# Kernel optimization log

Hardware: AMD Instinct MI355X
Metric: run time of the kernel (lower is better)

Reference implementation:

```python
import jax, jax.numpy as jnp
import numpy as np

D_MODEL = 2048
D_FF = 4 * D_MODEL  # 8192, GPT-2 MLP convention
TOTAL = D_MODEL * D_FF          # elements per weight matrix
L = TOTAL // 2                  # complex FFT length (real/imag interleaved pairs)
NUM_COEFFS = 16
BATCH, SEQ = 2, 4096


def _decompress(coeffs_real, coeffs_imag, indices, shape, scale):
    """Faithful port of FastPoincareFourier.decompress_matrix.
    Scatter K complex coeffs into a length-L zero buffer, ifft, then
    de-interleave real/imag back into a flat real vector of length 2L == TOTAL.
    """
    coeffs = jax.lax.complex(coeffs_real, coeffs_imag)
    full_fft = jnp.zeros((L,), dtype=jnp.complex64).at[indices].set(coeffs)
    restored = jnp.fft.ifft(full_fft)  # [L] complex
    # stack([real, imag], dim=1).flatten() -> interleaved [2L]
    flat = jnp.stack([jnp.real(restored), jnp.imag(restored)], axis=1).reshape(-1)
    # 2L == TOTAL exactly (TOTAL is even), so no trunc/pad needed
    return flat.reshape(shape) * scale  # scale broadcasts ([1])


def setup_inputs() -> dict:
    key = jax.random.key(0)
    ks = jax.random.split(key, 12)
    # coefficients scaled by L*0.02 so ifft (which divides by L) yields ~N(0,0.02) weights
    cscale = L * 0.02
    return {
        "x": jax.random.normal(ks[0], (BATCH, SEQ, D_MODEL), dtype=jnp.float32),
        "fc_coeffs_real": jax.random.normal(ks[1], (NUM_COEFFS,), dtype=jnp.float32) * cscale,
        "fc_coeffs_imag": jax.random.normal(ks[2], (NUM_COEFFS,), dtype=jnp.float32) * cscale,
        "fc_scale": jax.random.uniform(ks[3], (1,), dtype=jnp.float32) + 0.5,
        "proj_coeffs_real": jax.random.normal(ks[4], (NUM_COEFFS,), dtype=jnp.float32) * cscale,
        "proj_coeffs_imag": jax.random.normal(ks[5], (NUM_COEFFS,), dtype=jnp.float32) * cscale,
        "proj_scale": jax.random.uniform(ks[6], (1,), dtype=jnp.float32) + 0.5,
        "c_fc_bias": jax.random.normal(ks[7], (D_FF,), dtype=jnp.float32) * 0.02,
        "c_proj_bias": jax.random.normal(ks[8], (D_MODEL,), dtype=jnp.float32) * 0.02,
        "fc_indices": jax.random.randint(ks[9], (NUM_COEFFS,), 0, L, dtype=jnp.int64),
        "proj_indices": jax.random.randint(ks[10], (NUM_COEFFS,), 0, L, dtype=jnp.int64),
    }


def reference(x, fc_coeffs_real, fc_coeffs_imag, fc_scale,
              proj_coeffs_real, proj_coeffs_imag, proj_scale,
              c_fc_bias, c_proj_bias, fc_indices, proj_indices):
    # W_fc: [d_model, d_ff]; F.linear(x, W.T) == x @ W
    w_fc = _decompress(fc_coeffs_real, fc_coeffs_imag, fc_indices, (D_MODEL, D_FF), fc_scale)
    h = jnp.einsum('bsd,df->bsf', x, w_fc) + c_fc_bias
    h = jax.nn.gelu(h, approximate=False)  # nn.GELU() default = exact erf
    # W_proj: [d_ff, d_model]
    w_proj = _decompress(proj_coeffs_real, proj_coeffs_imag, proj_indices, (D_FF, D_MODEL), proj_scale)
    out = jnp.einsum('bsf,fd->bsd', h, w_proj) + c_proj_bias
    return out
```

## Files before the change

kernel.cpp:

```cpp
#include <hip/hip_runtime.h>
#include <stdint.h>


typedef short bfrag8 __attribute__((ext_vector_type(8)));
typedef short bfrag4 __attribute__((ext_vector_type(4)));
typedef float f32x4  __attribute__((ext_vector_type(4)));

#define LMASK 8388607u
#define TWO_PI_OVER_L 7.4901405658478575e-7f

__device__ __forceinline__ unsigned short f2bf(float f) {
    unsigned u = __float_as_uint(f);
    u = (u + 0x7FFFu + ((u >> 16) & 1u)) >> 16;
    return (unsigned short)u;
}
__device__ __forceinline__ float bf2f(unsigned short h) {
    unsigned u = ((unsigned)h) << 16;
    return __builtin_bit_cast(float, u);
}
__device__ __forceinline__ unsigned pk2bf(float a, float b) {
    unsigned ua = __float_as_uint(a) + 0x8000u;
    unsigned ub = __float_as_uint(b) + 0x8000u;
    return __builtin_amdgcn_perm(ub, ua, 0x07060302u);
}
__device__ __forceinline__ float gelu_fast(float x) {
    float xx = x * x;
    float p  = fmaf(xx, 0.044715f, 1.0f);
    float t  = (x * p) * -2.3022083f;
    float e  = __builtin_amdgcn_exp2f(t);
    return x * __builtin_amdgcn_rcpf(1.0f + e);
}
__device__ __forceinline__ void sc_ph(unsigned ph, float& sn, float& cs) {
    __sincosf((float)ph * TWO_PI_OVER_L, &sn, &cs);
}

#if defined(__has_builtin)
#if __has_builtin(__builtin_amdgcn_mfma_f32_16x16x16bf16_1k)
#define HAVE_MFMA16_1K 1
#endif
#endif
__device__ __forceinline__ void mfma16(f32x4& acc, bfrag4 a, bfrag4 b) {
#ifdef HAVE_MFMA16_1K
    acc = __builtin_amdgcn_mfma_f32_16x16x16bf16_1k(a, b, acc, 0, 0, 0);
#else
    asm("v_mfma_f32_16x16x16_bf16 %0, %1, %2, %0" : "+v"(acc) : "v"(a), "v"(b));
#endif
}

__device__ __forceinline__ bool keep_coef(const int* __restrict__ idx, int kk) {
    int v = idx[kk];
    bool keep = true;
    for (int j = kk + 1; j < 16; ++j) keep = keep && (idx[j] != v);
    return keep;
}

__global__ __launch_bounds__(512, 4) void k_t1(
    const float* __restrict__ x,
    const float* __restrict__ fcr, const float* __restrict__ fci,
    const int* __restrict__ fidx,  const float* __restrict__ fcs,
    unsigned short* __restrict__ t1)
{
    __shared__ float red[8 * 512];
    const int tid  = threadIdx.x;
    const int w    = tid >> 6;
    const int lane = tid & 63;
    const int lr   = lane & 15;
    const int hi   = lane >> 4;
    const size_t tok0 = (size_t)blockIdx.x * 16;

    const float sc = fcs[0] * (1.0f / 8388608.0f);
    const int p   = lr & 1;
    const int kk0 = lr >> 1, kk1 = 8 + (lr >> 1);
    unsigned s0, s1; float a0, b0, a1, b1;
    {
        bool k0 = keep_coef(fidx, kk0), k1 = keep_coef(fidx, kk1);
        s0 = (((unsigned)fidx[kk0]) << 12) & LMASK;
        s1 = (((unsigned)fidx[kk1]) << 12) & LMASK;
        a0 = k0 ? fcr[kk0] * sc : 0.f;  b0 = k0 ? fci[kk0] * sc : 0.f;
        a1 = k1 ? fcr[kk1] * sc : 0.f;  b1 = k1 ? fci[kk1] * sc : 0.f;
    }

    f32x4 acc[2];
    { f32x4 z = {0.f,0.f,0.f,0.f}; acc[0] = z; acc[1] = z; }
    #pragma unroll 2
    for (int s = 0; s < 8; ++s) {
        int k = w * 256 + s * 32 + hi * 8;
        const float* xp = x + (tok0 + lr) * 2048 + k;
        float4 v0 = *(const float4*)xp;
        float4 v1 = *(const float4*)(xp + 4);
        uint4 aw = make_uint4(pk2bf(v0.x, v0.y), pk2bf(v0.z, v0.w),
                              pk2bf(v1.x, v1.y), pk2bf(v1.z, v1.w));
        bfrag8 af = __builtin_bit_cast(bfrag8, aw);
        float e0[8], e1[8];
        #pragma unroll
        for (int t = 0; t < 8; ++t) {
            float sn, cs;
            sc_ph((s0 * (unsigned)(k + t)) & LMASK, sn, cs);
            e0[t] = p ? fmaf(a0, sn, b0 * cs) : fmaf(a0, cs, -b0 * sn);
            sc_ph((s1 * (unsigned)(k + t)) & LMASK, sn, cs);
            e1[t] = p ? fmaf(a1, sn, b1 * cs) : fmaf(a1, cs, -b1 * sn);
        }
        uint4 bw0 = make_uint4(pk2bf(e0[0], e0[1]), pk2bf(e0[2], e0[3]),
                               pk2bf(e0[4], e0[5]), pk2bf(e0[6], e0[7]));
        uint4 bw1 = make_uint4(pk2bf(e1[0], e1[1]), pk2bf(e1[2], e1[3]),
                               pk2bf(e1[4], e1[5]), pk2bf(e1[6], e1[7]));
        bfrag8 bf0 = __builtin_bit_cast(bfrag8, bw0);
        bfrag8 bf1 = __builtin_bit_cast(bfrag8, bw1);
        acc[0] = __builtin_amdgcn_mfma_f32_16x16x32_bf16(af, bf0, acc[0], 0, 0, 0);
        acc[1] = __builtin_amdgcn_mfma_f32_16x16x32_bf16(af, bf1, acc[1], 0, 0, 0);
    }
    #pragma unroll
    for (int nj = 0; nj < 2; ++nj)
        #pragma unroll
        for (int r = 0; r < 4; ++r)
            red[w * 512 + (hi * 4 + r) * 32 + nj * 16 + lr] = acc[nj][r];
    __syncthreads();
    float s = 0.f;
    #pragma unroll
    for (int w2 = 0; w2 < 8; ++w2) s += red[w2 * 512 + tid];
    t1[(size_t)blockIdx.x * 512 + tid] = f2bf(s);
}

__global__ __launch_bounds__(512, 4) void k_mid(
    const unsigned short* __restrict__ t1,
    const int* __restrict__ fidx,
    const int* __restrict__ pidx,
    const float* __restrict__ prr, const float* __restrict__ pri,
    const float* __restrict__ prs,
    const float* __restrict__ fcb,
    unsigned short* __restrict__ t2p)
{
    __shared__ float red[2 * 8 * 512];
    const int tid  = threadIdx.x;
    const int w    = tid >> 6;
    const int lane = tid & 63;
    const int lr   = lane & 15;
    const int hi   = lane >> 4;
    const int fc   = blockIdx.x;
    const int g0   = blockIdx.y * 16;
    const int fb_w = fc * 512 + w * 64;

    bfrag8 va0[2], va1[2];
    f32x4  cb0[2], cb1[2];
    unsigned skv[4];
    #pragma unroll
    for (int c = 0; c < 4; ++c) skv[c] = ((unsigned)fidx[hi * 4 + c]) & LMASK;
    #pragma unroll
    for (int sl = 0; sl < 2; ++sl) {
        #pragma unroll
        for (int rv = 0; rv < 2; ++rv) {
            int j = fb_w + sl * 32 + rv * 16 + lr;
            unsigned m = ((unsigned)j) >> 1;
            int pj = j & 1;
            float v[8];
            #pragma unroll
            for (int c = 0; c < 4; ++c) {
                float sn, cs;
                sc_ph((skv[c] * m) & LMASK, sn, cs);
                v[2 * c]     = pj ? sn : cs;
                v[2 * c + 1] = pj ? cs : -sn;
            }
            uint4 pw = make_uint4(pk2bf(v[0], v[1]), pk2bf(v[2], v[3]),
                                  pk2bf(v[4], v[5]), pk2bf(v[6], v[7]));
            if (rv == 0) va0[sl] = __builtin_bit_cast(bfrag8, pw);
            else         va1[sl] = __builtin_bit_cast(bfrag8, pw);
        }
        int fb = fb_w + sl * 32;
        cb0[sl] = *(const f32x4*)(fcb + fb + hi * 4);
        cb1[sl] = *(const f32x4*)(fcb + fb + 16 + hi * 4);
    }

    bfrag4 u00[2], u01[2], u10[2], u11[2];
    {
        const float scp = prs[0] * (1.0f / 8388608.0f);
        const int pp = lr & 1;
        #pragma unroll
        for (int rv = 0; rv < 2; ++rv) {
            int kk = rv * 8 + (lr >> 1);
            bool kp = keep_coef(pidx, kk);
            unsigned s = (((unsigned)pidx[kk]) << 10) & LMASK;
            float a = kp ? prr[kk] * scp : 0.f;
            float b = kp ? pri[kk] * scp : 0.f;
            #pragma unroll
            for (int sl = 0; sl < 2; ++sl) {
                #pragma unroll
                for (int hf = 0; hf < 2; ++hf) {
                    unsigned f0 = (unsigned)(fb_w + sl * 32 + hf * 16 + 4 * hi);
                    float v[4];
                    #pragma unroll
                    for (int t = 0; t < 4; ++t) {
                        float sn, cs;
                        sc_ph((s * (f0 + t)) & LMASK, sn, cs);
                        v[t] = pp ? fmaf(a, sn, b * cs) : fmaf(a, cs, -b * sn);
                    }
                    uint2 pw = make_uint2(pk2bf(v[0], v[1]), pk2bf(v[2], v[3]));
                    bfrag4 fr = __builtin_bit_cast(bfrag4, pw);
                    if      (rv == 0 && hf == 0) u00[sl] = fr;
                    else if (rv == 0 && hf == 1) u01[sl] = fr;
                    else if (rv == 1 && hf == 0) u10[sl] = fr;
                    else                         u11[sl] = fr;
                }
            }
        }
    }
    const int toff = lr * 32 + hi * 8;

    #pragma unroll 1
    for (int pi = 0; pi < 8; ++pi) {
        int ga = g0 + pi * 2, gb = ga + 1;
        bfrag8 tA = *(const bfrag8*)(t1 + (size_t)ga * 512 + toff);
        bfrag8 tB = *(const bfrag8*)(t1 + (size_t)gb * 512 + toff);
        f32x4 aA0 = {0.f,0.f,0.f,0.f}, aA1 = {0.f,0.f,0.f,0.f};
        f32x4 aB0 = {0.f,0.f,0.f,0.f}, aB1 = {0.f,0.f,0.f,0.f};
        #pragma unroll
        for (int sl = 0; sl < 2; ++sl) {
            f32x4 sA0 = __builtin_amdgcn_mfma_f32_16x16x32_bf16(va0[sl], tA, cb0[sl], 0, 0, 0);
            f32x4 sB0 = __builtin_amdgcn_mfma_f32_16x16x32_bf16(va0[sl], tB, cb0[sl], 0, 0, 0);
            f32x4 sA1 = __builtin_amdgcn_mfma_f32_16x16x32_bf16(va1[sl], tA, cb1[sl], 0, 0, 0);
            f32x4 sB1 = __builtin_amdgcn_mfma_f32_16x16x32_bf16(va1[sl], tB, cb1[sl], 0, 0, 0);
            uint2 hA0 = make_uint2(pk2bf(gelu_fast(sA0[0]), gelu_fast(sA0[1])),
                                   pk2bf(gelu_fast(sA0[2]), gelu_fast(sA0[3])));
            uint2 hB0 = make_uint2(pk2bf(gelu_fast(sB0[0]), gelu_fast(sB0[1])),
                                   pk2bf(gelu_fast(sB0[2]), gelu_fast(sB0[3])));
            uint2 hA1 = make_uint2(pk2bf(gelu_fast(sA1[0]), gelu_fast(sA1[1])),
                                   pk2bf(gelu_fast(sA1[2]), gelu_fast(sA1[3])));
            uint2 hB1 = make_uint2(pk2bf(gelu_fast(sB1[0]), gelu_fast(sB1[1])),
                                   pk2bf(gelu_fast(sB1[2]), gelu_fast(sB1[3])));
            bfrag4 fA0 = __builtin_bit_cast(bfrag4, hA0);
            bfrag4 fB0 = __builtin_bit_cast(bfrag4, hB0);
            bfrag4 fA1 = __builtin_bit_cast(bfrag4, hA1);
            bfrag4 fB1 = __builtin_bit_cast(bfrag4, hB1);
            mfma16(aA0, u00[sl], fA0);
            mfma16(aB0, u00[sl], fB0);
            mfma16(aA1, u10[sl], fA0);
            mfma16(aB1, u10[sl], fB0);
            mfma16(aA0, u01[sl], fA1);
            mfma16(aB0, u01[sl], fB1);
            mfma16(aA1, u11[sl], fA1);
            mfma16(aB1, u11[sl], fB1);
        }
        #pragma unroll
        for (int r = 0; r < 4; ++r) {
            int r2a = hi * 4 + r, r2b = 16 + hi * 4 + r;
            red[(0 * 8 + w) * 512 + lr * 32 + ((r2a + lr) & 31)] = aA0[r];
            red[(0 * 8 + w) * 512 + lr * 32 + ((r2b + lr) & 31)] = aA1[r];
            red[(1 * 8 + w) * 512 + lr * 32 + ((r2a + lr) & 31)] = aB0[r];
            red[(1 * 8 + w) * 512 + lr * 32 + ((r2b + lr) & 31)] = aB1[r];
        }
        __syncthreads();
        {
            int tok = tid >> 5, rr = tid & 31;
            int slot = tok * 32 + ((rr + tok) & 31);
            float sa = 0.f, sb = 0.f;
            #pragma unroll
            for (int w2 = 0; w2 < 8; ++w2) {
                sa += red[(0 * 8 + w2) * 512 + slot];
                sb += red[(1 * 8 + w2) * 512 + slot];
            }
            t2p[((size_t)fc * 512 + ga) * 512 + tid] = f2bf(sa);
            t2p[((size_t)fc * 512 + gb) * 512 + tid] = f2bf(sb);
        }
        __syncthreads();
    }
}

__global__ __launch_bounds__(512, 4) void k_out(
    const unsigned short* __restrict__ t2p,
    const int* __restrict__ pidx,
    const float* __restrict__ prb,
    float* __restrict__ out)
{
    __shared__ unsigned short lT[512];
    const int tid  = threadIdx.x;
    const int w    = tid >> 6;
    const int lane = tid & 63;
    const int lr   = lane & 15;
    const int hi   = lane >> 4;
    const int g    = blockIdx.x;
    const size_t tok0 = (size_t)g * 16;

    {
        float s = 0.f;
        #pragma unroll
        for (int c = 0; c < 16; ++c)
            s += bf2f(t2p[((size_t)c * 512 + g) * 512 + tid]);
        lT[tid] = f2bf(s);
    }
    unsigned skv[4];
    #pragma unroll
    for (int c = 0; c < 4; ++c) skv[c] = ((unsigned)pidx[hi * 4 + c]) & LMASK;
    __syncthreads();
    const bfrag8 t2a = *(const bfrag8*)(lT + lr * 32 + hi * 8);
    #pragma unroll 4
    for (int nj = 0; nj < 16; ++nj) {
        int d = w * 256 + nj * 16 + lr;
        unsigned m = ((unsigned)d) >> 1;
        int pd = d & 1;
        float v[8];
        #pragma unroll
        for (int c = 0; c < 4; ++c) {
            float sn, cs;
            sc_ph((skv[c] * m) & LMASK, sn, cs);
            v[2 * c]     = pd ? sn : cs;
            v[2 * c + 1] = pd ? cs : -sn;
        }
        uint4 pw = make_uint4(pk2bf(v[0], v[1]), pk2bf(v[2], v[3]),
                              pk2bf(v[4], v[5]), pk2bf(v[6], v[7]));
        bfrag8 vp = __builtin_bit_cast(bfrag8, pw);
        float bn = prb[d];
        f32x4 c4 = {bn, bn, bn, bn};
        f32x4 o = __builtin_amdgcn_mfma_f32_16x16x32_bf16(t2a, vp, c4, 0, 0, 0);
        #pragma unroll
        for (int r = 0; r < 4; ++r)
            out[(tok0 + hi * 4 + r) * 2048 + d] = o[r];
    }
}

extern "C" void kernel_launch(void* const* d_in, const int* in_sizes, int n_in,
                              void* d_out, int out_size, void* d_ws, size_t ws_size,
                              hipStream_t stream) {
    (void)in_sizes; (void)n_in; (void)out_size; (void)ws_size;
    const float* x   = (const float*)d_in[0];
    const float* fcr = (const float*)d_in[1];
    const float* fci = (const float*)d_in[2];
    const float* fcs = (const float*)d_in[3];
    const float* prr = (const float*)d_in[4];
    const float* pri = (const float*)d_in[5];
    const float* prs = (const float*)d_in[6];
    const float* fcb = (const float*)d_in[7];
    const float* prb = (const float*)d_in[8];
    const int* fidx  = (const int*)d_in[9];
    const int* pidx  = (const int*)d_in[10];
    float* out = (float*)d_out;
    char* ws = (char*)d_ws;

    size_t off = 0;
    auto take = [&](size_t bytes) { size_t p = off; off = (off + bytes + 255) & ~(size_t)255; return p; };
    unsigned short* t1  = (unsigned short*)(ws + take((size_t)8192 * 32 * 2));
    unsigned short* t2p = (unsigned short*)(ws + take((size_t)16 * 8192 * 32 * 2));

    k_t1 <<<dim3(512),    512, 0, stream>>>(x, fcr, fci, fidx, fcs, t1);
    k_mid<<<dim3(16, 32), 512, 0, stream>>>(t1, fidx, pidx, prr, pri, prs, fcb, t2p);
    k_out<<<dim3(512),    512, 0, stream>>>(t2p, pidx, prb, out);
}
```

Before: 76.90 us.

## Stage fc/proj basis in LDS and split tokens across waves in k_mid

k_mid now computes the fc and proj Fourier basis fragments once per block into shared memory, with padded rows. Each wave then owns two token groups and loops over all 512 ff columns, replacing the per-wave column split that needed a cross-wave LDS reduction and two barriers per iteration. This removes the reduction traffic and synchronisation. In exchange it adds LDS reads in the inner loop, uses more shared memory, and lowers the launch-bounds occupancy hint from 4 to 2.

```diff
diff --git a/kernel.cpp b/kernel.cpp
--- a/kernel.cpp
+++ b/kernel.cpp
@@ -121,7 +121,7 @@
     t1[(size_t)blockIdx.x * 512 + tid] = f2bf(s);
 }
 
-__global__ __launch_bounds__(512, 4) void k_mid(
+__global__ __launch_bounds__(512, 2) void k_mid(
     const unsigned short* __restrict__ t1,
     const int* __restrict__ fidx,
     const int* __restrict__ pidx,
@@ -130,137 +130,86 @@
     const float* __restrict__ fcb,
     unsigned short* __restrict__ t2p)
 {
-    __shared__ float red[2 * 8 * 512];
+    __shared__ __align__(16) unsigned short vfc[512 * 32];
+    __shared__ __align__(16) unsigned short upr[32 * 520];
+    __shared__ float lbias[512];
     const int tid  = threadIdx.x;
     const int w    = tid >> 6;
     const int lane = tid & 63;
     const int lr   = lane & 15;
     const int hi   = lane >> 4;
     const int fc   = blockIdx.x;
-    const int g0   = blockIdx.y * 16;
-    const int fb_w = fc * 512 + w * 64;
-
-    bfrag8 va0[2], va1[2];
-    f32x4  cb0[2], cb1[2];
-    unsigned skv[4];
-    #pragma unroll
-    for (int c = 0; c < 4; ++c) skv[c] = ((unsigned)fidx[hi * 4 + c]) & LMASK;
-    #pragma unroll
-    for (int sl = 0; sl < 2; ++sl) {
-        #pragma unroll
-        for (int rv = 0; rv < 2; ++rv) {
-            int j = fb_w + sl * 32 + rv * 16 + lr;
-            unsigned m = ((unsigned)j) >> 1;
-            int pj = j & 1;
-            float v[8];
-            #pragma unroll
-            for (int c = 0; c < 4; ++c) {
-                float sn, cs;
-                sc_ph((skv[c] * m) & LMASK, sn, cs);
-                v[2 * c]     = pj ? sn : cs;
-                v[2 * c + 1] = pj ? cs : -sn;
-            }
-            uint4 pw = make_uint4(pk2bf(v[0], v[1]), pk2bf(v[2], v[3]),
-                                  pk2bf(v[4], v[5]), pk2bf(v[6], v[7]));
-            if (rv == 0) va0[sl] = __builtin_bit_cast(bfrag8, pw);
-            else         va1[sl] = __builtin_bit_cast(bfrag8, pw);
-        }
-        int fb = fb_w + sl * 32;
-        cb0[sl] = *(const f32x4*)(fcb + fb + hi * 4);
-        cb1[sl] = *(const f32x4*)(fcb + fb + 16 + hi * 4);
-    }
-
-    bfrag4 u00[2], u01[2], u10[2], u11[2];
+
+    {
+        int jg = fc * 512 + tid;
+        unsigned m = ((unsigned)jg) >> 1;
+        int pj = jg & 1;
+        unsigned short* row = vfc + tid * 32;
+        #pragma unroll
+        for (int k = 0; k < 16; ++k) {
+            float sn, cs;
+            sc_ph(((((unsigned)fidx[k]) & LMASK) * m) & LMASK, sn, cs);
+            row[2 * k]     = f2bf(pj ? sn : cs);
+            row[2 * k + 1] = f2bf(pj ? cs : -sn);
+        }
+    }
     {
         const float scp = prs[0] * (1.0f / 8388608.0f);
-        const int pp = lr & 1;
-        #pragma unroll
-        for (int rv = 0; rv < 2; ++rv) {
-            int kk = rv * 8 + (lr >> 1);
-            bool kp = keep_coef(pidx, kk);
-            unsigned s = (((unsigned)pidx[kk]) << 10) & LMASK;
-            float a = kp ? prr[kk] * scp : 0.f;
-            float b = kp ? pri[kk] * scp : 0.f;
-            #pragma unroll
-            for (int sl = 0; sl < 2; ++sl) {
-                #pragma unroll
-                for (int hf = 0; hf < 2; ++hf) {
-                    unsigned f0 = (unsigned)(fb_w + sl * 32 + hf * 16 + 4 * hi);
-                    float v[4];
-                    #pragma unroll
-                    for (int t = 0; t < 4; ++t) {
-                        float sn, cs;
-                        sc_ph((s * (f0 + t)) & LMASK, sn, cs);
-                        v[t] = pp ? fmaf(a, sn, b * cs) : fmaf(a, cs, -b * sn);
-                    }
-                    uint2 pw = make_uint2(pk2bf(v[0], v[1]), pk2bf(v[2], v[3]));
-                    bfrag4 fr = __builtin_bit_cast(bfrag4, pw);
-                    if      (rv == 0 && hf == 0) u00[sl] = fr;
-                    else if (rv == 0 && hf == 1) u01[sl] = fr;
-                    else if (rv == 1 && hf == 0) u10[sl] = fr;
-                    else                         u11[sl] = fr;
-                }
-            }
-        }
-    }
+        int k  = tid >> 5;
+        int f0 = (tid & 31) * 16;
+        bool kp = keep_coef(pidx, k);
+        unsigned s = (((unsigned)pidx[k]) << 10) & LMASK;
+        float a = kp ? prr[k] * scp : 0.f;
+        float b = kp ? pri[k] * scp : 0.f;
+        unsigned short* r0 = upr + (2 * k) * 520 + f0;
+        unsigned short* r1 = upr + (2 * k + 1) * 520 + f0;
+        unsigned fg = (unsigned)(fc * 512 + f0);
+        #pragma unroll
+        for (int t = 0; t < 16; ++t) {
+            float sn, cs;
+            sc_ph((s * (fg + t)) & LMASK, sn, cs);
+            r0[t] = f2bf(fmaf(a, cs, -b * sn));
+            r1[t] = f2bf(fmaf(a, sn, b * cs));
+        }
+    }
+    lbias[tid] = fcb[fc * 512 + tid];
+    __syncthreads();
+
+    const int ga = blockIdx.y * 16 + w * 2, gb = ga + 1;
     const int toff = lr * 32 + hi * 8;
-
-    #pragma unroll 1
-    for (int pi = 0; pi < 8; ++pi) {
-        int ga = g0 + pi * 2, gb = ga + 1;
-        bfrag8 tA = *(const bfrag8*)(t1 + (size_t)ga * 512 + toff);
-        bfrag8 tB = *(const bfrag8*)(t1 + (size_t)gb * 512 + toff);
-        f32x4 aA0 = {0.f,0.f,0.f,0.f}, aA1 = {0.f,0.f,0.f,0.f};
-        f32x4 aB0 = {0.f,0.f,0.f,0.f}, aB1 = {0.f,0.f,0.f,0.f};
-        #pragma unroll
-        for (int sl = 0; sl < 2; ++sl) {
-            f32x4 sA0 = __builtin_amdgcn_mfma_f32_16x16x32_bf16(va0[sl], tA, cb0[sl], 0, 0, 0);
-            f32x4 sB0 = __builtin_amdgcn_mfma_f32_16x16x32_bf16(va0[sl], tB, cb0[sl], 0, 0, 0);
-            f32x4 sA1 = __builtin_amdgcn_mfma_f32_16x16x32_bf16(va1[sl], tA, cb1[sl], 0, 0, 0);
-            f32x4 sB1 = __builtin_amdgcn_mfma_f32_16x16x32_bf16(va1[sl], tB, cb1[sl], 0, 0, 0);
-            uint2 hA0 = make_uint2(pk2bf(gelu_fast(sA0[0]), gelu_fast(sA0[1])),
-                                   pk2bf(gelu_fast(sA0[2]), gelu_fast(sA0[3])));
-            uint2 hB0 = make_uint2(pk2bf(gelu_fast(sB0[0]), gelu_fast(sB0[1])),
-                                   pk2bf(gelu_fast(sB0[2]), gelu_fast(sB0[3])));
-            uint2 hA1 = make_uint2(pk2bf(gelu_fast(sA1[0]), gelu_fast(sA1[1])),
-                                   pk2bf(gelu_fast(sA1[2]), gelu_fast(sA1[3])));
-            uint2 hB1 = make_uint2(pk2bf(gelu_fast(sB1[0]), gelu_fast(sB1[1])),
-                                   pk2bf(gelu_fast(sB1[2]), gelu_fast(sB1[3])));
-            bfrag4 fA0 = __builtin_bit_cast(bfrag4, hA0);
-            bfrag4 fB0 = __builtin_bit_cast(bfrag4, hB0);
-            bfrag4 fA1 = __builtin_bit_cast(bfrag4, hA1);
-            bfrag4 fB1 = __builtin_bit_cast(bfrag4, hB1);
-            mfma16(aA0, u00[sl], fA0);
-            mfma16(aB0, u00[sl], fB0);
-            mfma16(aA1, u10[sl], fA0);
-            mfma16(aB1, u10[sl], fB0);
-            mfma16(aA0, u01[sl], fA1);
-            mfma16(aB0, u01[sl], fB1);
-            mfma16(aA1, u11[sl], fA1);
-            mfma16(aB1, u11[sl], fB1);
-        }
-        #pragma unroll
-        for (int r = 0; r < 4; ++r) {
-            int r2a = hi * 4 + r, r2b = 16 + hi * 4 + r;
-            red[(0 * 8 + w) * 512 + lr * 32 + ((r2a + lr) & 31)] = aA0[r];
-            red[(0 * 8 + w) * 512 + lr * 32 + ((r2b + lr) & 31)] = aA1[r];
-            red[(1 * 8 + w) * 512 + lr * 32 + ((r2a + lr) & 31)] = aB0[r];
-            red[(1 * 8 + w) * 512 + lr * 32 + ((r2b + lr) & 31)] = aB1[r];
-        }
-        __syncthreads();
-        {
-            int tok = tid >> 5, rr = tid & 31;
-            int slot = tok * 32 + ((rr + tok) & 31);
-            float sa = 0.f, sb = 0.f;
-            #pragma unroll
-            for (int w2 = 0; w2 < 8; ++w2) {
-                sa += red[(0 * 8 + w2) * 512 + slot];
-                sb += red[(1 * 8 + w2) * 512 + slot];
-            }
-            t2p[((size_t)fc * 512 + ga) * 512 + tid] = f2bf(sa);
-            t2p[((size_t)fc * 512 + gb) * 512 + tid] = f2bf(sb);
-        }
-        __syncthreads();
+    const bfrag8 tA = *(const bfrag8*)(t1 + (size_t)ga * 512 + toff);
+    const bfrag8 tB = *(const bfrag8*)(t1 + (size_t)gb * 512 + toff);
+    f32x4 aA0 = {0.f,0.f,0.f,0.f}, aA1 = {0.f,0.f,0.f,0.f};
+    f32x4 aB0 = {0.f,0.f,0.f,0.f}, aB1 = {0.f,0.f,0.f,0.f};
+
+    #pragma unroll 2
+    for (int it = 0; it < 32; ++it) {
+        const int f0 = it * 16;
+        bfrag8 va = *(const bfrag8*)(vfc + (f0 + lr) * 32 + hi * 8);
+        f32x4 cbv = *(const f32x4*)(lbias + f0 + hi * 4);
+        f32x4 sA = __builtin_amdgcn_mfma_f32_16x16x32_bf16(va, tA, cbv, 0, 0, 0);
+        f32x4 sB = __builtin_amdgcn_mfma_f32_16x16x32_bf16(va, tB, cbv, 0, 0, 0);
+        uint2 hwA = make_uint2(pk2bf(gelu_fast(sA[0]), gelu_fast(sA[1])),
+                               pk2bf(gelu_fast(sA[2]), gelu_fast(sA[3])));
+        uint2 hwB = make_uint2(pk2bf(gelu_fast(sB[0]), gelu_fast(sB[1])),
+                               pk2bf(gelu_fast(sB[2]), gelu_fast(sB[3])));
+        bfrag4 hA = __builtin_bit_cast(bfrag4, hwA);
+        bfrag4 hB = __builtin_bit_cast(bfrag4, hwB);
+        bfrag4 u0 = *(const bfrag4*)(upr + lr * 520 + f0 + hi * 4);
+        bfrag4 u1 = *(const bfrag4*)(upr + (16 + lr) * 520 + f0 + hi * 4);
+        mfma16(aA0, u0, hA);
+        mfma16(aA1, u1, hA);
+        mfma16(aB0, u0, hB);
+        mfma16(aB1, u1, hB);
+    }
+
+    {
+        unsigned short* oa = t2p + ((size_t)fc * 512 + ga) * 512;
+        unsigned short* ob = t2p + ((size_t)fc * 512 + gb) * 512;
+        *(uint2*)(oa + lr * 32 + hi * 4)      = make_uint2(pk2bf(aA0[0], aA0[1]), pk2bf(aA0[2], aA0[3]));
+        *(uint2*)(oa + lr * 32 + 16 + hi * 4) = make_uint2(pk2bf(aA1[0], aA1[1]), pk2bf(aA1[2], aA1[3]));
+        *(uint2*)(ob + lr * 32 + hi * 4)      = make_uint2(pk2bf(aB0[0], aB0[1]), pk2bf(aB0[2], aB0[3]));
+        *(uint2*)(ob + lr * 32 + 16 + hi * 4) = make_uint2(pk2bf(aB1[0], aB1[1]), pk2bf(aB1[2], aB1[3]));
     }
 }
 
```

Result: faster. 69.95 us (-9.0%).
